# Performance work log

Measured on AMD Instinct MI355X. Metric: run time of the kernel, lower is better.

The kernel has to match this reference:

```python
import jax, jax.numpy as jnp
import numpy as np

DECAY = 0.5
COEFF = 0.05
INH_C = 2.0
SPARSE_THRES = 0.9


def setup_inputs() -> dict:
    key = jax.random.key(0)
    k1, k2 = jax.random.split(key)
    x = jax.random.normal(k1, (1, 512, 448, 448), dtype=jnp.float32)
    # small-magnitude boost weights (buffer starts at zero in torch but we
    # use nonzero values so the mv / inhibition path is exercised)
    boost_weight = jax.random.normal(k2, (512, 512), dtype=jnp.float32) * 0.01
    return {"x": x, "boost_weight": boost_weight}


def reference(x, boost_weight):
    # x: [1, C, H, W]; boost_weight: [C, C]
    x_avr = jnp.mean(x[0], axis=(1, 2))                      # [C] adaptive avgpool(1) + squeeze
    boost_vec = boost_weight @ x_avr                          # [C]
    inh_value = jnp.mean(boost_vec)
    x_tmp = jax.nn.relu(x_avr + boost_vec - INH_C * inh_value)
    threshold = jnp.max(x_tmp) * SPARSE_THRES
    x_sparse = jnp.where(x_tmp < threshold, 0.0, x_tmp)      # masked_fill

    # Hebbian update (torch commit_update, done under no_grad):
    weight_tmp = jnp.outer(x_tmp, x_sparse)                  # [C, C]
    C = weight_tmp.shape[0]
    weight_tmp = weight_tmp * (1.0 - jnp.eye(C, dtype=weight_tmp.dtype))  # fill_diagonal_(0)
    norm = jnp.linalg.norm(weight_tmp)
    weight_tmp = jnp.where(
        jnp.isfinite(norm) & (norm > 0), weight_tmp / norm, weight_tmp
    )
    new_boost_weight = boost_weight * DECAY + COEFF * weight_tmp

    # gated channel rescale of the full tensor
    scale = (x_tmp / (x_avr + 1e-12)).reshape(1, -1, 1, 1)
    out = x * scale                                          # [1, C, H, W]
    return out, new_boost_weight
```

## Files before the change

### kernel.cpp

```cpp
#include <hip/hip_runtime.h>
#include <math.h>

#define NCH    512
#define HW     200704
#define HW4    50176
#define GROUPS 8
#define G4     6272
#define X_ELEMS 102760448ULL

#define WS_XTMP  4096
#define WS_XSP   4608
#define WS_SCALE 5120
#define WS_INV   5632

typedef float vf4 __attribute__((ext_vector_type(4)));

__global__ __launch_bounds__(256) void k_mean_partial(const float* __restrict__ x,
                                                      float* __restrict__ ws) {
    __shared__ float red[4];
    const int g = blockIdx.x;
    const int c = blockIdx.y;
    const float4* xv = reinterpret_cast<const float4*>(x) + (size_t)c * HW4 + (size_t)g * G4;
    float s = 0.f;
    for (int i = threadIdx.x; i < G4; i += 256) {
        float4 v = xv[i];
        s += (v.x + v.y) + (v.z + v.w);
    }
    #pragma unroll
    for (int o = 32; o > 0; o >>= 1) s += __shfl_down(s, o, 64);
    const int wave = threadIdx.x >> 6;
    const int lane = threadIdx.x & 63;
    if (lane == 0) red[wave] = s;
    __syncthreads();
    if (threadIdx.x == 0) {
        ws[g * NCH + c] = (red[0] + red[1]) + (red[2] + red[3]);
    }
}

__global__ __launch_bounds__(512) void k_stats(const float* __restrict__ W,
                                               float* __restrict__ ws) {
    __shared__ float avr[512];
    __shared__ float red[8];
    __shared__ float redA[8], redB[8], redD[8];
    __shared__ float bcast;

    const int t = threadIdx.x;
    const int wave = t >> 6;
    const int lane = t & 63;

    {
        float s = 0.f;
        #pragma unroll
        for (int g = 0; g < GROUPS; ++g) s += ws[g * NCH + t];
        avr[t] = s * (1.0f / (float)HW);
    }
    __syncthreads();

    float acc = 0.f;
    const float* row = W + (size_t)t * NCH;
    #pragma unroll 8
    for (int j = 0; j < NCH; ++j) acc += row[j] * avr[j];

    float s = acc;
    #pragma unroll
    for (int o = 32; o > 0; o >>= 1) s += __shfl_down(s, o, 64);
    if (lane == 0) red[wave] = s;
    __syncthreads();
    if (t == 0) {
        float tt = 0.f;
        #pragma unroll
        for (int w = 0; w < 8; ++w) tt += red[w];
        bcast = tt * (1.0f / (float)NCH);
    }
    __syncthreads();
    const float inh = bcast;

    float xtmp = avr[t] + acc - 2.0f * inh;
    xtmp = xtmp > 0.f ? xtmp : 0.f;

    float m = xtmp;
    #pragma unroll
    for (int o = 32; o > 0; o >>= 1) m = fmaxf(m, __shfl_down(m, o, 64));
    __syncthreads();
    if (lane == 0) red[wave] = m;
    __syncthreads();
    if (t == 0) {
        float mm = red[0];
        #pragma unroll
        for (int w = 1; w < 8; ++w) mm = fmaxf(mm, red[w]);
        bcast = mm * 0.9f;
    }
    __syncthreads();
    const float thr = bcast;
    const float xs = (xtmp < thr) ? 0.f : xtmp;

    float a = xtmp * xtmp;
    float b = xs * xs;
    float d = xtmp * xs; d = d * d;
    #pragma unroll
    for (int o = 32; o > 0; o >>= 1) {
        a += __shfl_down(a, o, 64);
        b += __shfl_down(b, o, 64);
        d += __shfl_down(d, o, 64);
    }
    if (lane == 0) { redA[wave] = a; redB[wave] = b; redD[wave] = d; }
    __syncthreads();
    if (t == 0) {
        float s1 = 0.f, s2 = 0.f, s3 = 0.f;
        #pragma unroll
        for (int w = 0; w < 8; ++w) { s1 += redA[w]; s2 += redB[w]; s3 += redD[w]; }
        float n2 = s1 * s2 - s3;
        float norm = (n2 > 0.f) ? sqrtf(n2) : 0.f;
        float inv = (norm > 0.f && isfinite(norm)) ? (1.0f / norm) : 1.0f;
        ws[WS_INV] = inv;
    }

    ws[WS_XTMP + t]  = xtmp;
    ws[WS_XSP + t]   = xs;
    ws[WS_SCALE + t] = xtmp / (avr[t] + 1e-12f);
}

__global__ __launch_bounds__(256) void k_tail(const float* __restrict__ x,
                                              const float* __restrict__ W,
                                              const float* __restrict__ ws,
                                              float* __restrict__ out,
                                              float* __restrict__ outW) {
    const int bid = blockIdx.x;
    if (bid < 1024) {
        const int idx = bid * 256 + threadIdx.x;
        const int i = idx >> 9;
        const int j = idx & (NCH - 1);
        const float inv = ws[WS_INV];
        const float v = (i == j) ? 0.f : ws[WS_XTMP + i] * ws[WS_XSP + j] * inv;
        outW[idx] = 0.5f * W[idx] + 0.05f * v;
    } else {
        const int b = bid - 1024;
        const int c_lin = b / 49;
        const int t = b - c_lin * 49;
        const int c = (NCH - 1) - c_lin;
        const float s = ws[WS_SCALE + c];
        const size_t chan_base = (size_t)c * HW4;
        const int base = t * 1024 + threadIdx.x;
        const float4* xv = reinterpret_cast<const float4*>(x);
        float4* ov = reinterpret_cast<float4*>(out);
        #pragma unroll
        for (int k = 0; k < 4; ++k) {
            const size_t off = chan_base + (size_t)(base + k * 256);
            float4 v = xv[off];
            v.x *= s; v.y *= s; v.z *= s; v.w *= s;
            __builtin_nontemporal_store(*(const vf4*)&v, (vf4*)&ov[off]);
        }
    }
}

extern "C" void kernel_launch(void* const* d_in, const int* in_sizes, int n_in,
                              void* d_out, int out_size, void* d_ws, size_t ws_size,
                              hipStream_t stream) {
    const float* x = (const float*)d_in[0];
    const float* W = (const float*)d_in[1];
    float* out  = (float*)d_out;
    float* outW = out + X_ELEMS;
    float* ws   = (float*)d_ws;

    dim3 grid_mean(GROUPS, NCH);
    k_mean_partial<<<grid_mean, 256, 0, stream>>>(x, ws);
    k_stats<<<1, 512, 0, stream>>>(W, ws);
    k_tail<<<1024 + 49 * NCH, 256, 0, stream>>>(x, W, ws, out, outW);
}
```

Measured before the change: 758.6 us.

## Fuse pipeline into single cooperative kernel with per-channel blocks and reverse reread

Replaces the three-kernel sequence with one cooperative kernel where each block owns a channel, computes the mean, syncs the grid, computes the boost mat-vec row, then derives statistics redundantly per block. The rescale pass rereads the channel in reverse order so recently read data may still be in cache. This removes launch gaps and the intermediate stats kernel, but only 512 blocks run, so occupancy is low for a bandwidth-bound stream and grid syncs add cost. The old path stays as a fallback if the cooperative launch fails.

```diff
diff --git a/kernel.cpp b/kernel.cpp
--- a/kernel.cpp
+++ b/kernel.cpp
@@ -1,19 +1,145 @@
 #include <hip/hip_runtime.h>
+#include <hip/hip_cooperative_groups.h>
 #include <math.h>
 
-#define NCH    512
-#define HW     200704
-#define HW4    50176
+namespace cg = cooperative_groups;
+
+#define NCH     512
+#define HW      200704
+#define HW4     50176
+#define X_ELEMS 102760448ULL
+#define CITERS  196
+
+typedef float vf4 __attribute__((ext_vector_type(4)));
+
+__device__ __forceinline__ float block_reduce_sum256(float v, float* red) {
+    #pragma unroll
+    for (int o = 32; o > 0; o >>= 1) v += __shfl_down(v, o, 64);
+    const int wave = threadIdx.x >> 6;
+    const int lane = threadIdx.x & 63;
+    if (lane == 0) red[wave] = v;
+    __syncthreads();
+    float r = (red[0] + red[1]) + (red[2] + red[3]);
+    __syncthreads();
+    return r;
+}
+
+__device__ __forceinline__ float block_reduce_max256(float v, float* red) {
+    #pragma unroll
+    for (int o = 32; o > 0; o >>= 1) v = fmaxf(v, __shfl_down(v, o, 64));
+    const int wave = threadIdx.x >> 6;
+    const int lane = threadIdx.x & 63;
+    if (lane == 0) red[wave] = v;
+    __syncthreads();
+    float r = fmaxf(fmaxf(red[0], red[1]), fmaxf(red[2], red[3]));
+    __syncthreads();
+    return r;
+}
+
+__global__ __launch_bounds__(256, 2) void k_coop(const float* __restrict__ x,
+                                                 const float* __restrict__ W,
+                                                 float* __restrict__ ws,
+                                                 float* __restrict__ out,
+                                                 float* __restrict__ outW) {
+    __shared__ float red[4];
+    __shared__ float avr_s[NCH];
+    __shared__ float bv_s[NCH];
+    __shared__ float xt_s[NCH];
+    __shared__ float xs_s[NCH];
+    cg::grid_group grid = cg::this_grid();
+
+    const int c = blockIdx.x;
+    const int t = threadIdx.x;
+    const float4* xv = reinterpret_cast<const float4*>(x) + (size_t)c * HW4;
+
+    {
+        float s0 = 0.f, s1 = 0.f, s2 = 0.f, s3 = 0.f;
+        for (int i = 0; i < CITERS; i += 4) {
+            float4 a = xv[(size_t)(i + 0) * 256 + t];
+            float4 b = xv[(size_t)(i + 1) * 256 + t];
+            float4 cc = xv[(size_t)(i + 2) * 256 + t];
+            float4 d = xv[(size_t)(i + 3) * 256 + t];
+            s0 += (a.x + a.y) + (a.z + a.w);
+            s1 += (b.x + b.y) + (b.z + b.w);
+            s2 += (cc.x + cc.y) + (cc.z + cc.w);
+            s3 += (d.x + d.y) + (d.z + d.w);
+        }
+        float ssum = block_reduce_sum256((s0 + s1) + (s2 + s3), red);
+        if (t == 0) ws[c] = ssum * (1.0f / (float)HW);
+    }
+    grid.sync();
+
+    {
+        #pragma unroll
+        for (int j = t; j < NCH; j += 256) avr_s[j] = ws[j];
+        __syncthreads();
+        const float* row = W + (size_t)c * NCH;
+        float acc = row[t] * avr_s[t] + row[t + 256] * avr_s[t + 256];
+        float bv = block_reduce_sum256(acc, red);
+        if (t == 0) ws[NCH + c] = bv;
+    }
+    grid.sync();
+
+    #pragma unroll
+    for (int j = t; j < NCH; j += 256) bv_s[j] = ws[NCH + j];
+    __syncthreads();
+
+    const float a0 = avr_s[t],       a1 = avr_s[t + 256];
+    const float bv0 = bv_s[t],       bv1 = bv_s[t + 256];
+
+    const float inh = block_reduce_sum256(bv0 + bv1, red) * (1.0f / (float)NCH);
+    float xt0 = fmaxf(a0 + bv0 - 2.0f * inh, 0.f);
+    float xt1 = fmaxf(a1 + bv1 - 2.0f * inh, 0.f);
+
+    const float thr = block_reduce_max256(fmaxf(xt0, xt1), red) * 0.9f;
+    const float xs0 = (xt0 < thr) ? 0.f : xt0;
+    const float xs1 = (xt1 < thr) ? 0.f : xt1;
+
+    const float sa = block_reduce_sum256(xt0 * xt0 + xt1 * xt1, red);
+    const float sb = block_reduce_sum256(xs0 * xs0 + xs1 * xs1, red);
+    const float d0 = xt0 * xs0, d1 = xt1 * xs1;
+    const float sd = block_reduce_sum256(d0 * d0 + d1 * d1, red);
+    const float n2 = sa * sb - sd;
+    const float norm = (n2 > 0.f) ? sqrtf(n2) : 0.f;
+    const float inv = (norm > 0.f && isfinite(norm)) ? (1.0f / norm) : 1.0f;
+
+    xt_s[t] = xt0; xt_s[t + 256] = xt1;
+    xs_s[t] = xs0; xs_s[t + 256] = xs1;
+    __syncthreads();
+
+    {
+        const float xtc = xt_s[c];
+        const float* wrow = W + (size_t)c * NCH;
+        float* orow = outW + (size_t)c * NCH;
+        #pragma unroll
+        for (int j = t; j < NCH; j += 256) {
+            const float v = (j == c) ? 0.f : xtc * xs_s[j] * inv;
+            orow[j] = 0.5f * wrow[j] + 0.05f * v;
+        }
+    }
+
+    {
+        const float s = xt_s[c] / (avr_s[c] + 1e-12f);
+        float4* ov = reinterpret_cast<float4*>(out) + (size_t)c * HW4;
+        for (int i = CITERS - 2; i >= 0; i -= 2) {
+            const size_t o1 = (size_t)(i + 1) * 256 + t;
+            const size_t o0 = (size_t)i * 256 + t;
+            float4 a = xv[o1];
+            float4 b = xv[o0];
+            a.x *= s; a.y *= s; a.z *= s; a.w *= s;
+            b.x *= s; b.y *= s; b.z *= s; b.w *= s;
+            __builtin_nontemporal_store(*(const vf4*)&a, (vf4*)&ov[o1]);
+            __builtin_nontemporal_store(*(const vf4*)&b, (vf4*)&ov[o0]);
+        }
+    }
+}
+
 #define GROUPS 8
 #define G4     6272
-#define X_ELEMS 102760448ULL
-
 #define WS_XTMP  4096
 #define WS_XSP   4608
 #define WS_SCALE 5120
 #define WS_INV   5632
-
-typedef float vf4 __attribute__((ext_vector_type(4)));
 
 __global__ __launch_bounds__(256) void k_mean_partial(const float* __restrict__ x,
                                                       float* __restrict__ ws) {
@@ -32,9 +158,7 @@
     const int lane = threadIdx.x & 63;
     if (lane == 0) red[wave] = s;
     __syncthreads();
-    if (threadIdx.x == 0) {
-        ws[g * NCH + c] = (red[0] + red[1]) + (red[2] + red[3]);
-    }
+    if (threadIdx.x == 0) ws[g * NCH + c] = (red[0] + red[1]) + (red[2] + red[3]);
 }
 
 __global__ __launch_bounds__(512) void k_stats(const float* __restrict__ W,
@@ -111,8 +235,7 @@
         for (int w = 0; w < 8; ++w) { s1 += redA[w]; s2 += redB[w]; s3 += redD[w]; }
         float n2 = s1 * s2 - s3;
         float norm = (n2 > 0.f) ? sqrtf(n2) : 0.f;
-        float inv = (norm > 0.f && isfinite(norm)) ? (1.0f / norm) : 1.0f;
-        ws[WS_INV] = inv;
+        ws[WS_INV] = (norm > 0.f && isfinite(norm)) ? (1.0f / norm) : 1.0f;
     }
 
     ws[WS_XTMP + t]  = xtmp;
@@ -162,6 +285,13 @@
     float* outW = out + X_ELEMS;
     float* ws   = (float*)d_ws;
 
+    void* args[] = {(void*)&x, (void*)&W, (void*)&ws, (void*)&out, (void*)&outW};
+    hipError_t e = hipLaunchCooperativeKernel((void*)k_coop, dim3(NCH), dim3(256),
+                                              args, 0, stream);
+    if (e == hipSuccess) return;
+
+    (void)hipGetLastError();
+
     dim3 grid_mean(GROUPS, NCH);
     k_mean_partial<<<grid_mean, 256, 0, stream>>>(x, ws);
     k_stats<<<1, 512, 0, stream>>>(W, ws);
```

Result: slower. 845.9 us (+11.5%).
